# Kernel optimization log

Measured on AMD Instinct MI355X. Metric: run time of the kernel, lower is better.

## Reference

```python
import jax, jax.numpy as jnp
from jax import lax
import numpy as np

N, T, F, H, L, TOPK = 2048, 64, 16, 64, 16, 10


def setup_inputs() -> dict:
    key = jax.random.key(0)
    ks = jax.random.split(key, 12)
    s_ih = 1.0 / np.sqrt(H)
    inp = {
        "x": jax.random.normal(ks[0], (N, T, F), dtype=jnp.float32),
        # GRU params (torch layout: weight_ih_l0 (3H,F), weight_hh_l0 (3H,H))
        "W_ih": jax.random.uniform(ks[1], (3 * H, F), minval=-s_ih, maxval=s_ih),
        "W_hh": jax.random.uniform(ks[2], (3 * H, H), minval=-s_ih, maxval=s_ih),
        "b_ih": jax.random.uniform(ks[3], (3 * H,), minval=-s_ih, maxval=s_ih),
        "b_hh": jax.random.uniform(ks[4], (3 * H,), minval=-s_ih, maxval=s_ih),
        "Wq": jax.random.normal(ks[5], (H, H)) * (1.0 / np.sqrt(H)),
        "Wk": jax.random.normal(ks[6], (H, H)) * (1.0 / np.sqrt(H)),
        "W1": jax.random.normal(ks[7], (F, F)) * (1.0 / np.sqrt(F)),
        "b1": jnp.zeros((F,), jnp.float32),
        "W2": jax.random.normal(ks[8], (1, F)) * (1.0 / np.sqrt(F)),
        "b2": jnp.zeros((1,), jnp.float32),
    }
    return inp


def _gru(x, W_ih, W_hh, b_ih, b_hh):
    # x: (N, T, F) -> hidden states (N, T, H)
    xp = x @ W_ih.T + b_ih  # precompute input gates: (N, T, 3H)

    def step(h, xt):
        gh = h @ W_hh.T + b_hh
        xr, xz, xn = jnp.split(xt, 3, axis=-1)
        hr, hz, hn = jnp.split(gh, 3, axis=-1)
        r = jax.nn.sigmoid(xr + hr)
        z = jax.nn.sigmoid(xz + hz)
        n = jnp.tanh(xn + r * hn)
        h_new = (1.0 - z) * n + z * h
        return h_new, h_new

    h0 = jnp.zeros((x.shape[0], W_hh.shape[1]), x.dtype)
    _, hs = lax.scan(step, h0, jnp.swapaxes(xp, 0, 1))  # (T, N, H)
    return jnp.swapaxes(hs, 0, 1)


def reference(x, W_ih, W_hh, b_ih, b_hh, Wq, Wk, W1, b1, W2, b2):
    n, t, f = x.shape
    h = _gru(x, W_ih, W_hh, b_ih, b_hh)          # (N, T, H)
    queries = h[:, -1, :] @ Wq.T                 # (N, H)
    keys = h[:, -L:, :] @ Wk.T                   # (N, L, H)
    # cross-sample scores: query i vs key (stock m, lag l)
    scores = jnp.einsum("nh,mlh->nml", queries, keys)  # (N, N, L)
    eye = jnp.eye(n, dtype=bool)[:, :, None]
    scores = jnp.where(eye, jnp.float32(-1e9), scores)
    flat = scores.reshape(n, n * L)
    topk_vals, topk_idx = lax.top_k(flat, TOPK)  # order differs from torch sorted=False but math is permutation-invariant
    leader_idx = topk_idx // L                   # (N, k)
    lag_idx = topk_idx % L
    time_idx = t - (L - lag_idx)
    leader_feats = x[leader_idx, time_idx]       # (N, k, F)
    w = jax.nn.softmax(topk_vals, axis=1)
    weighted = jnp.sum(leader_feats * w[..., None], axis=1)  # (N, F)
    hid = jax.nn.leaky_relu(weighted @ W1.T + b1, negative_slope=0.01)
    out = (hid @ W2.T + b2).reshape(-1)          # (N,)
    return out
```

## Files before the change

### kernel.cpp

```cpp
#include <hip/hip_runtime.h>

#define NN 2048
#define TT 64
#define FF 16
#define HH 64
#define LL 16
#define TOPKK 10
#define CAP 960

#define AS 72
#define XAS 40
#define XPS 196

typedef __bf16 bf16x8 __attribute__((ext_vector_type(8)));
typedef float floatx4 __attribute__((ext_vector_type(4)));

union FragCast { uint4 u; bf16x8 b; unsigned short s[8]; };
union Pack4 { unsigned short s[4]; uint2 u; };

__device__ __forceinline__ unsigned short f2bf(float f) {
    unsigned u = __float_as_uint(f);
    return (unsigned short)((u + 0x7fff + ((u >> 16) & 1)) >> 16);
}
__device__ __forceinline__ float bf2f(unsigned short h) {
    return __uint_as_float(((unsigned)h) << 16);
}
__device__ __forceinline__ void split3(float v, unsigned short& a, unsigned short& b, unsigned short& c) {
    a = f2bf(v); float r = v - bf2f(a);
    b = f2bf(r); float r2 = r - bf2f(b);
    c = f2bf(r2);
}
__device__ __forceinline__ float fsigmoid(float x) {
    return __builtin_amdgcn_rcpf(1.f + __builtin_amdgcn_exp2f(-1.442695041f * x));
}
__device__ __forceinline__ float ftanh(float x) {
    return 1.f - 2.f * __builtin_amdgcn_rcpf(1.f + __builtin_amdgcn_exp2f(2.885390082f * x));
}
__device__ __forceinline__ void async_copy16(const void* g, void* l) {
    __builtin_amdgcn_global_load_lds(
        (const __attribute__((address_space(1))) unsigned int*)g,
        (__attribute__((address_space(3))) unsigned int*)l, 16, 0, 0);
}
#define MFMA16(A, B, C) __builtin_amdgcn_mfma_f32_16x16x32_bf16((A), (B), (C), 0, 0, 0)

__global__ __launch_bounds__(256, 2) void gru_kernel(
    const float* __restrict__ x,
    const float* __restrict__ W_ih,
    const float* __restrict__ W_hh,
    const float* __restrict__ b_ih,
    const float* __restrict__ b_hh,
    float* __restrict__ h_tail,
    int* __restrict__ cnt)
{
    __shared__ __attribute__((aligned(16))) unsigned short Asp[2][3][16 * AS];
    __shared__ __attribute__((aligned(16))) unsigned short xa[3][16 * XAS];
    __shared__ __attribute__((aligned(16))) float xp[16 * XPS];
    __shared__ __attribute__((aligned(16))) float x_lds[4 * TT * FF];

    const int t    = threadIdx.x;
    const int wv   = t >> 6;
    const int lane = t & 63;
    const int nh   = lane & 15;
    const int quad = lane >> 4;
    const int n0   = blockIdx.x * 4;

    if (t < 4) cnt[blockIdx.x * 4 + t] = 0;

    {
        const char* src = (const char*)(x + (size_t)n0 * TT * FF);
        char* dst = (char*)x_lds;
#pragma unroll
        for (int i = 0; i < 4; ++i)
            async_copy16(src + i * 4096 + t * 16, dst + i * 4096 + t * 16);
    }
    {
        unsigned* p = (unsigned*)&Asp[0][0][0];
        for (int i = t; i < 2 * 3 * 16 * AS / 2; i += 256) p[i] = 0;
        unsigned* q = (unsigned*)&xa[0][0];
        for (int i = t; i < 3 * 16 * XAS / 2; i += 256) q[i] = 0;
    }

    const int jb = wv * 16 + nh;
    const float brz = b_ih[jb] + b_hh[jb];
    const float bz  = b_ih[64 + jb] + b_hh[64 + jb];
    const float bxn = b_ih[128 + jb];
    const float bhn = b_hh[128 + jb];

    bf16x8 wf[3][2][3];
#pragma unroll
    for (int nt = 0; nt < 3; ++nt) {
        const int gr = (wv + 4 * nt) * 16 + nh;
#pragma unroll
        for (int kc = 0; kc < 2; ++kc) {
            const float* p = W_hh + gr * 64 + kc * 32 + quad * 8;
            FragCast f1, f2, f3;
#pragma unroll
            for (int i = 0; i < 8; ++i) split3(p[i], f1.s[i], f2.s[i], f3.s[i]);
            wf[nt][kc][0] = f1.b; wf[nt][kc][1] = f2.b; wf[nt][kc][2] = f3.b;
        }
    }
    bf16x8 wfi[3][3];
#pragma unroll
    for (int nt = 0; nt < 3; ++nt) {
        const int gr = (wv + 4 * nt) * 16 + nh;
        FragCast f1, f2, f3;
#pragma unroll
        for (int i = 0; i < 8; ++i) {
            const float v = (quad < 2) ? W_ih[gr * 16 + quad * 8 + i] : 0.f;
            split3(v, f1.s[i], f2.s[i], f3.s[i]);
        }
        wfi[nt][0] = f1.b; wfi[nt][1] = f2.b; wfi[nt][2] = f3.b;
    }

    __syncthreads();

    float hprev = 0.f;

    for (int chunk = 0; chunk < 16; ++chunk) {
        {
            const int row = t >> 4, f = t & 15;
            const int p = row & 3, sl = row >> 2;
            const float xv = x_lds[p * (TT * FF) + (chunk * 4 + sl) * FF + f];
            unsigned short a, b, c; split3(xv, a, b, c);
            xa[0][row * XAS + f] = a;
            xa[1][row * XAS + f] = b;
            xa[2][row * XAS + f] = c;
        }
        __syncthreads();
        {
            floatx4 xA0 = {0,0,0,0}, xB0 = {0,0,0,0};
            floatx4 xA1 = {0,0,0,0}, xB1 = {0,0,0,0};
            floatx4 xA2 = {0,0,0,0}, xB2 = {0,0,0,0};
            const int aoff = nh * XAS + quad * 8;
            FragCast a1, a2, a3;
            a1.u = *(const uint4*)&xa[0][aoff];
            a2.u = *(const uint4*)&xa[1][aoff];
            a3.u = *(const uint4*)&xa[2][aoff];
            xA0 = MFMA16(a1.b, wfi[0][0], xA0); xA1 = MFMA16(a1.b, wfi[1][0], xA1); xA2 = MFMA16(a1.b, wfi[2][0], xA2);
            xB0 = MFMA16(a1.b, wfi[0][1], xB0); xB1 = MFMA16(a1.b, wfi[1][1], xB1); xB2 = MFMA16(a1.b, wfi[2][1], xB2);
            xB0 = MFMA16(a2.b, wfi[0][0], xB0); xB1 = MFMA16(a2.b, wfi[1][0], xB1); xB2 = MFMA16(a2.b, wfi[2][0], xB2);
            xA0 = MFMA16(a1.b, wfi[0][2], xA0); xA1 = MFMA16(a1.b, wfi[1][2], xA1); xA2 = MFMA16(a1.b, wfi[2][2], xA2);
            xA0 = MFMA16(a2.b, wfi[0][1], xA0); xA1 = MFMA16(a2.b, wfi[1][1], xA1); xA2 = MFMA16(a2.b, wfi[2][1], xA2);
            xB0 = MFMA16(a3.b, wfi[0][0], xB0); xB1 = MFMA16(a3.b, wfi[1][0], xB1); xB2 = MFMA16(a3.b, wfi[2][0], xB2);
#pragma unroll
            for (int r = 0; r < 4; ++r) {
                const int m = quad * 4 + r;
                xp[m * XPS + (wv + 0) * 16 + nh] = xA0[r] + xB0[r];
                xp[m * XPS + (wv + 4) * 16 + nh] = xA1[r] + xB1[r];
                xp[m * XPS + (wv + 8) * 16 + nh] = xA2[r] + xB2[r];
            }
        }
        __syncthreads();

#pragma unroll
        for (int si = 0; si < 4; ++si) {
            const int step = chunk * 4 + si;
            const int rb = step & 1, wb = rb ^ 1;
            floatx4 aA0 = {0,0,0,0}, aB0 = {0,0,0,0};
            floatx4 aA1 = {0,0,0,0}, aB1 = {0,0,0,0};
            floatx4 aA2 = {0,0,0,0}, aB2 = {0,0,0,0};
#pragma unroll
            for (int kc = 0; kc < 2; ++kc) {
                const int aoff = nh * AS + kc * 32 + quad * 8;
                FragCast a1, a2, a3;
                a1.u = *(const uint4*)&Asp[rb][0][aoff];
                a2.u = *(const uint4*)&Asp[rb][1][aoff];
                a3.u = *(const uint4*)&Asp[rb][2][aoff];
                aA0 = MFMA16(a1.b, wf[0][kc][0], aA0); aA1 = MFMA16(a1.b, wf[1][kc][0], aA1); aA2 = MFMA16(a1.b, wf[2][kc][0], aA2);
                aB0 = MFMA16(a1.b, wf[0][kc][1], aB0); aB1 = MFMA16(a1.b, wf[1][kc][1], aB1); aB2 = MFMA16(a1.b, wf[2][kc][1], aB2);
                aB0 = MFMA16(a2.b, wf[0][kc][0], aB0); aB1 = MFMA16(a2.b, wf[1][kc][0], aB1); aB2 = MFMA16(a2.b, wf[2][kc][0], aB2);
                aA0 = MFMA16(a1.b, wf[0][kc][2], aA0); aA1 = MFMA16(a1.b, wf[1][kc][2], aA1); aA2 = MFMA16(a1.b, wf[2][kc][2], aA2);
                aA0 = MFMA16(a2.b, wf[0][kc][1], aA0); aA1 = MFMA16(a2.b, wf[1][kc][1], aA1); aA2 = MFMA16(a2.b, wf[2][kc][1], aA2);
                aB0 = MFMA16(a3.b, wf[0][kc][0], aB0); aB1 = MFMA16(a3.b, wf[1][kc][0], aB1); aB2 = MFMA16(a3.b, wf[2][kc][0], aB2);
            }
            {
                const int xrow = si * 4 + quad;
                const float xr = xp[xrow * XPS + jb];
                const float xz = xp[xrow * XPS + 64 + jb];
                const float xn = xp[xrow * XPS + 128 + jb];
                const float rgt = fsigmoid((aA0[0] + aB0[0]) + xr + brz);
                const float zgt = fsigmoid((aA1[0] + aB1[0]) + xz + bz);
                const float ngt = ftanh((xn + bxn) + rgt * ((aA2[0] + aB2[0]) + bhn));
                const float h  = (1.f - zgt) * ngt + zgt * hprev;
                hprev = h;
                unsigned short la, lb2, lc; split3(h, la, lb2, lc);
                const int ho = (4 * quad) * AS + jb;
                Asp[wb][0][ho] = la;
                Asp[wb][1][ho] = lb2;
                Asp[wb][2][ho] = lc;
                if (step >= TT - LL)
                    h_tail[((size_t)(n0 + quad) * LL + (step - (TT - LL))) * HH + jb] = h;
            }
            __syncthreads();
        }
    }
}

__global__ __launch_bounds__(256, 2) void prep_kernel(
    const float* __restrict__ h_tail,
    const float* __restrict__ Wk,
    const float* __restrict__ Wq,
    float* __restrict__ Kmat,
    unsigned short* __restrict__ Kh,
    float* __restrict__ Qf,
    unsigned short* __restrict__ Qh)
{
    __shared__ __attribute__((aligned(16))) float Wk_s[64 * 68];
    __shared__ __attribute__((aligned(16))) float Wq_s[64 * 69];
    __shared__ __attribute__((aligned(16))) float h_s[64 * 68];

    const int t = threadIdx.x;
    const size_t rbase = (size_t)blockIdx.x * 64;

#pragma unroll
    for (int k = 0; k < 4; ++k) {
        const int idx = t + k * 256;
        const int j = idx >> 4, ci = idx & 15;
        *(float4*)(h_s + j * 68 + ci * 4) = *(const float4*)(h_tail + (rbase + j) * 64 + ci * 4);
    }
    for (int c = t; c < 1024; c += 256) {
        const int j = c >> 4, ci = c & 15;
        *(float4*)(Wk_s + j * 68 + ((ci ^ (j >> 2)) << 2)) = *(const float4*)(Wk + c * 4);
    }
    for (int c = t; c < 4096; c += 256) {
        const int j = c >> 6, i = c & 63;
        Wq_s[j * 69 + i] = Wq[c];
    }
    __syncthreads();

    const int rg = t >> 4;
    const int cg = t & 15;
    float acc[4][4];
#pragma unroll
    for (int r = 0; r < 4; ++r)
#pragma unroll
        for (int c = 0; c < 4; ++c) acc[r][c] = 0.f;

#pragma unroll
    for (int ci = 0; ci < 16; ++ci) {
        float4 wv[4];
#pragma unroll
        for (int c = 0; c < 4; ++c) {
            const int j = cg * 4 + c;
            wv[c] = *(const float4*)(Wk_s + j * 68 + ((ci ^ cg) << 2));
        }
#pragma unroll
        for (int r = 0; r < 4; ++r) {
            const float4 hv = *(const float4*)(h_s + (rg * 4 + r) * 68 + ci * 4);
#pragma unroll
            for (int c = 0; c < 4; ++c)
                acc[r][c] += hv.x * wv[c].x + hv.y * wv[c].y
                           + hv.z * wv[c].z + hv.w * wv[c].w;
        }
    }
#pragma unroll
    for (int r = 0; r < 4; ++r) {
        const size_t row = rbase + rg * 4 + r;
        float4 o; o.x = acc[r][0]; o.y = acc[r][1]; o.z = acc[r][2]; o.w = acc[r][3];
        *(float4*)(Kmat + row * 64 + cg * 4) = o;
        Pack4 p;
#pragma unroll
        for (int c = 0; c < 4; ++c) p.s[c] = f2bf(acc[r][c]);
        *(uint2*)(Kh + row * 64 + cg * 4) = p.u;
    }

    {
        const int s = t >> 6, j = t & 63;
        const float* hr = h_s + (s * 16 + 15) * 68;
        float a0 = 0.f, a1 = 0.f;
#pragma unroll
        for (int i = 0; i < 64; i += 2) {
            a0 += hr[i] * Wq_s[j * 69 + i];
            a1 += hr[i + 1] * Wq_s[j * 69 + i + 1];
        }
        const float a = a0 + a1;
        const size_t qi = (size_t)(blockIdx.x * 4 + s) * 64 + j;
        Qf[qi] = a;
        Qh[qi] = f2bf(a);
    }
}

__global__ __launch_bounds__(512, 4) void score_kernel(
    const unsigned short* __restrict__ Kh,
    const unsigned short* __restrict__ Qh,
    int* __restrict__ cnt,
    int* __restrict__ ids)
{
    __shared__ float stat_s[8][4][16];
    __shared__ float stat_q[8][4][16];
    __shared__ float th_s[64];

    const int t    = threadIdx.x;
    const int wave = t >> 6;
    const int lane = t & 63;
    const int n    = lane & 15;
    const int quad = lane >> 4;

    const int qgroup = blockIdx.x >> 4;
    const int split  = blockIdx.x & 15;
    const int tile0  = split * 128 + wave * 16;

    FragCast bq[4][2];
#pragma unroll
    for (int qs = 0; qs < 4; ++qs) {
        const int qg = qgroup * 64 + qs * 16 + n;
        bq[qs][0].u = *(const uint4*)(Qh + (size_t)qg * 64 + quad * 8);
        bq[qs][1].u = *(const uint4*)(Qh + (size_t)qg * 64 + 32 + quad * 8);
    }

    float ssum[4] = {0.f,0.f,0.f,0.f}, ssq[4] = {0.f,0.f,0.f,0.f};
    for (int i = 0; i < 8; ++i) {
        const unsigned short* r = Kh + (size_t)((tile0 + i) * 16 + n) * 64;
        FragCast a0, a1;
        a0.u = *(const uint4*)(r + quad * 8);
        a1.u = *(const uint4*)(r + 32 + quad * 8);
#pragma unroll
        for (int qs = 0; qs < 4; ++qs) {
            floatx4 acc = {0.f, 0.f, 0.f, 0.f};
            acc = MFMA16(a0.b, bq[qs][0].b, acc);
            acc = MFMA16(a1.b, bq[qs][1].b, acc);
#pragma unroll
            for (int j = 0; j < 4; ++j) { ssum[qs] += acc[j]; ssq[qs] += acc[j] * acc[j]; }
        }
    }
#pragma unroll
    for (int qs = 0; qs < 4; ++qs) {
        ssum[qs] += __shfl_xor(ssum[qs], 16, 64); ssq[qs] += __shfl_xor(ssq[qs], 16, 64);
        ssum[qs] += __shfl_xor(ssum[qs], 32, 64); ssq[qs] += __shfl_xor(ssq[qs], 32, 64);
    }
    if (lane < 16) {
#pragma unroll
        for (int qs = 0; qs < 4; ++qs) { stat_s[wave][qs][n] = ssum[qs]; stat_q[wave][qs][n] = ssq[qs]; }
    }
    __syncthreads();
    if (t < 64) {
        const int qs = t >> 4, c = t & 15;
        float S = 0.f, S2 = 0.f;
#pragma unroll
        for (int w = 0; w < 8; ++w) { S += stat_s[w][qs][c]; S2 += stat_q[w][qs][c]; }
        const float inv = 1.f / 1024.f;
        const float mu = S * inv;
        float var = S2 * inv - mu * mu;
        var = var > 0.f ? var : 0.f;
        th_s[t] = mu + 2.6f * __fsqrt_rn(var);
    }
    __syncthreads();
    float th[4];
#pragma unroll
    for (int qs = 0; qs < 4; ++qs) th[qs] = th_s[qs * 16 + n];

    {
        FragCast a0, a1, na0, na1;
        const unsigned short* r0 = Kh + (size_t)(tile0 * 16 + n) * 64;
        a0.u = *(const uint4*)(r0 + quad * 8);
        a1.u = *(const uint4*)(r0 + 32 + quad * 8);
        for (int i = 0; i < 16; ++i) {
            if (i + 1 < 16) {
                const unsigned short* r = Kh + (size_t)((tile0 + i + 1) * 16 + n) * 64;
                na0.u = *(const uint4*)(r + quad * 8);
                na1.u = *(const uint4*)(r + 32 + quad * 8);
            }
            const int rowb = (tile0 + i) * 16 + quad * 4;
#pragma unroll
            for (int qs = 0; qs < 4; ++qs) {
                floatx4 acc = {0.f, 0.f, 0.f, 0.f};
                acc = MFMA16(a0.b, bq[qs][0].b, acc);
                acc = MFMA16(a1.b, bq[qs][1].b, acc);
                const int qg = qgroup * 64 + qs * 16 + n;
#pragma unroll
                for (int j = 0; j < 4; ++j) {
                    const float s = acc[j];
                    const int rowid = rowb + j;
                    if (s > th[qs] && (rowid >> 4) != qg) {
                        const int slot = atomicAdd(&cnt[qg], 1);
                        if (slot < CAP) ids[(size_t)qg * CAP + slot] = rowid;
                    }
                }
            }
            a0 = na0; a1 = na1;
        }
    }
}

__global__ __launch_bounds__(512) void final_kernel(
    const float* __restrict__ x,
    const float* __restrict__ Qf,
    const float* __restrict__ Kmat,
    const int* __restrict__ cnt,
    const int* __restrict__ ids,
    const float* __restrict__ W1, const float* __restrict__ b1,
    const float* __restrict__ W2, const float* __restrict__ b2,
    float* __restrict__ out)
{
    const int t    = threadIdx.x;
    const int w    = t >> 6;
    const int lane = t & 63;
    const int grp  = lane >> 4;
    const int sl   = lane & 15;
    const int q    = blockIdx.x * 8 + w;

    const int mc0 = cnt[q];
    const int mc  = mc0 < CAP ? mc0 : CAP;
    const float4 qv = *(const float4*)(Qf + (size_t)q * 64 + sl * 4);
    const int* idq = ids + (size_t)q * CAP;

    float v[TOPKK]; int vid[TOPKK];
#pragma unroll
    for (int r = 0; r < TOPKK; ++r) { v[r] = -3e38f; vid[r] = -1; }
    float vmin = -3e38f; int imin = 0;

    for (int c = grp; c < mc; c += 4) {
        const int id = idq[c];
        const float4 kv = *(const float4*)(Kmat + (size_t)id * 64 + sl * 4);
        float p = qv.x * kv.x + qv.y * kv.y + qv.z * kv.z + qv.w * kv.w;
        p += __shfl_xor(p, 1, 64);
        p += __shfl_xor(p, 2, 64);
        p += __shfl_xor(p, 4, 64);
        p += __shfl_xor(p, 8, 64);
        if (sl == 0 && p > vmin) {
#pragma unroll
            for (int r = 0; r < TOPKK; ++r) if (r == imin) { v[r] = p; vid[r] = id; }
            vmin = v[0]; imin = 0;
#pragma unroll
            for (int r = 1; r < TOPKK; ++r) if (v[r] < vmin) { vmin = v[r]; imin = r; }
        }
    }

    float topv[TOPKK]; int topi[TOPKK];
    unsigned used = 0;
    for (int r = 0; r < TOPKK; ++r) {
        float bv = -3e38f; int bi = -1, bs = -1;
#pragma unroll
        for (int s = 0; s < TOPKK; ++s)
            if (!((used >> s) & 1) && v[s] > bv) { bv = v[s]; bi = vid[s]; bs = s; }
        const float mybv = bv; const int mybi = bi;
#pragma unroll
        for (int st = 16; st <= 32; st <<= 1) {
            const float ov = __shfl_xor(bv, st, 64);
            const int   oi = __shfl_xor(bi, st, 64);
            if (ov > bv || (ov == bv && oi > bi)) { bv = ov; bi = oi; }
        }
        topv[r] = bv; topi[r] = bi;
        if (bs >= 0 && mybv == bv && mybi == bi) used |= (1u << bs);
    }
#pragma unroll
    for (int r = 0; r < TOPKK; ++r) {
        topv[r] = __shfl(topv[r], 0, 64);
        topi[r] = __shfl(topi[r], 0, 64);
    }

    float mx = topv[0];
#pragma unroll
    for (int r = 1; r < TOPKK; ++r) mx = topv[r] > mx ? topv[r] : mx;
    float wgt[TOPKK]; float sw = 0.f;
#pragma unroll
    for (int r = 0; r < TOPKK; ++r) {
        wgt[r] = (topi[r] >= 0) ? __expf(topv[r] - mx) : 0.f;
        sw += wgt[r];
    }
    const float inv = 1.f / sw;

    float4 f0 = {0,0,0,0}, f1 = {0,0,0,0}, f2 = {0,0,0,0}, f3 = {0,0,0,0};
    if (lane < TOPKK && topi[lane] >= 0) {
        const int wi = topi[lane];
        const float* xr = x + ((size_t)(wi >> 4) * TT + 48 + (wi & 15)) * FF;
        const float s = wgt[lane] * inv;
        float4 a = *(const float4*)(xr);
        float4 b = *(const float4*)(xr + 4);
        float4 cc = *(const float4*)(xr + 8);
        float4 d = *(const float4*)(xr + 12);
        f0.x = s * a.x; f0.y = s * a.y; f0.z = s * a.z; f0.w = s * a.w;
        f1.x = s * b.x; f1.y = s * b.y; f1.z = s * b.z; f1.w = s * b.w;
        f2.x = s * cc.x; f2.y = s * cc.y; f2.z = s * cc.z; f2.w = s * cc.w;
        f3.x = s * d.x; f3.y = s * d.y; f3.z = s * d.z; f3.w = s * d.w;
    }
#pragma unroll
    for (int st = 1; st <= 8; st <<= 1) {
        f0.x += __shfl_xor(f0.x, st, 64); f0.y += __shfl_xor(f0.y, st, 64);
        f0.z += __shfl_xor(f0.z, st, 64); f0.w += __shfl_xor(f0.w, st, 64);
        f1.x += __shfl_xor(f1.x, st, 64); f1.y += __shfl_xor(f1.y, st, 64);
        f1.z += __shfl_xor(f1.z, st, 64); f1.w += __shfl_xor(f1.w, st, 64);
        f2.x += __shfl_xor(f2.x, st, 64); f2.y += __shfl_xor(f2.y, st, 64);
        f2.z += __shfl_xor(f2.z, st, 64); f2.w += __shfl_xor(f2.w, st, 64);
        f3.x += __shfl_xor(f3.x, st, 64); f3.y += __shfl_xor(f3.y, st, 64);
        f3.z += __shfl_xor(f3.z, st, 64); f3.w += __shfl_xor(f3.w, st, 64);
    }

    float o = 0.f;
    if (lane < 16) {
        const float* w1r = W1 + lane * 16;
        float hh = b1[lane]
            + f0.x * w1r[0]  + f0.y * w1r[1]  + f0.z * w1r[2]  + f0.w * w1r[3]
            + f1.x * w1r[4]  + f1.y * w1r[5]  + f1.z * w1r[6]  + f1.w * w1r[7]
            + f2.x * w1r[8]  + f2.y * w1r[9]  + f2.z * w1r[10] + f2.w * w1r[11]
            + f3.x * w1r[12] + f3.y * w1r[13] + f3.z * w1r[14] + f3.w * w1r[15];
        hh = hh > 0.f ? hh : 0.01f * hh;
        o = hh * W2[lane];
    }
#pragma unroll
    for (int st = 1; st <= 8; st <<= 1) o += __shfl_xor(o, st, 64);
    if (lane == 0) out[q] = o + b2[0];
}

extern "C" void kernel_launch(void* const* d_in, const int* in_sizes, int n_in,
                              void* d_out, int out_size, void* d_ws, size_t ws_size,
                              hipStream_t stream) {
    const float* x    = (const float*)d_in[0];
    const float* W_ih = (const float*)d_in[1];
    const float* W_hh = (const float*)d_in[2];
    const float* b_ih = (const float*)d_in[3];
    const float* b_hh = (const float*)d_in[4];
    const float* Wq   = (const float*)d_in[5];
    const float* Wk   = (const float*)d_in[6];
    const float* W1   = (const float*)d_in[7];
    const float* b1   = (const float*)d_in[8];
    const float* W2   = (const float*)d_in[9];
    const float* b2   = (const float*)d_in[10];
    float* outp = (float*)d_out;
    (void)ws_size; (void)n_in; (void)in_sizes; (void)out_size;

    float* h_tail        = (float*)d_ws;
    int*   ids           = (int*)d_ws;
    float* Kmat          = h_tail + (size_t)2048 * 1024;
    unsigned short* Kh   = (unsigned short*)(Kmat + (size_t)32768 * 64);
    float* Qf            = (float*)(Kh + (size_t)32768 * 64);
    unsigned short* Qh   = (unsigned short*)(Qf + (size_t)2048 * 64);
    int*   cnt           = (int*)(Qh + (size_t)2048 * 64);

    gru_kernel<<<NN / 4, 256, 0, stream>>>(x, W_ih, W_hh, b_ih, b_hh, h_tail, cnt);
    prep_kernel<<<512, 256, 0, stream>>>(h_tail, Wk, Wq, Kmat, Kh, Qf, Qh);
    score_kernel<<<512, 512, 0, stream>>>(Kh, Qh, cnt, ids);
    final_kernel<<<NN / 8, 512, 0, stream>>>(x, Qf, Kmat, cnt, ids, W1, b1, W2, b2, outp);
}
```

Before: 256.7 us.

## Fuse K/Q projection into GRU kernel and prefetch keys in final kernel

The separate prep kernel is folded into the GRU kernel. The last 16 hidden states stay in a shared-memory arena and the Wk/Wq projections are computed in place, which removes a launch and the h_tail round trip through global memory. The LDS is unified into one 64000-byte arena so the projection can reuse the GRU buffers. This may limit occupancy to the declared two blocks per CU. The final kernel now uses 256-thread blocks and software-prefetches the next candidate's key id and vector to hide gather latency.

Result: no change. 255.2 us (-0.6%).

```diff
diff --git a/kernel.cpp b/kernel.cpp
--- a/kernel.cpp
+++ b/kernel.cpp
@@ -49,13 +49,22 @@
     const float* __restrict__ W_hh,
     const float* __restrict__ b_ih,
     const float* __restrict__ b_hh,
-    float* __restrict__ h_tail,
+    const float* __restrict__ Wk,
+    const float* __restrict__ Wq,
+    float* __restrict__ Kmat,
+    unsigned short* __restrict__ Kh,
+    float* __restrict__ Qf,
+    unsigned short* __restrict__ Qh,
     int* __restrict__ cnt)
 {
-    __shared__ __attribute__((aligned(16))) unsigned short Asp[2][3][16 * AS];
-    __shared__ __attribute__((aligned(16))) unsigned short xa[3][16 * XAS];
-    __shared__ __attribute__((aligned(16))) float xp[16 * XPS];
-    __shared__ __attribute__((aligned(16))) float x_lds[4 * TT * FF];
+    __shared__ __attribute__((aligned(16))) char arena[64000];
+    unsigned short* const Asp0 = (unsigned short*)arena;
+    unsigned short* const xa0  = (unsigned short*)(arena + 13824);
+    float* const xp            = (float*)(arena + 17664);
+    float* const x_lds         = (float*)(arena + 30208);
+    float* const h_keep        = (float*)(arena + 46592);
+#define ASP(b, l, i) Asp0[((b) * 3 + (l)) * (16 * AS) + (i)]
+#define XA(l, i)     xa0[(l) * (16 * XAS) + (i)]
 
     const int t    = threadIdx.x;
     const int wv   = t >> 6;
@@ -74,10 +83,10 @@
             async_copy16(src + i * 4096 + t * 16, dst + i * 4096 + t * 16);
     }
     {
-        unsigned* p = (unsigned*)&Asp[0][0][0];
-        for (int i = t; i < 2 * 3 * 16 * AS / 2; i += 256) p[i] = 0;
-        unsigned* q = (unsigned*)&xa[0][0];
-        for (int i = t; i < 3 * 16 * XAS / 2; i += 256) q[i] = 0;
+        unsigned* p = (unsigned*)Asp0;
+        for (int i = t; i < 3456; i += 256) p[i] = 0;
+        unsigned* q = (unsigned*)xa0;
+        for (int i = t; i < 960; i += 256) q[i] = 0;
     }
 
     const int jb = wv * 16 + nh;
@@ -122,9 +131,9 @@
             const int p = row & 3, sl = row >> 2;
             const float xv = x_lds[p * (TT * FF) + (chunk * 4 + sl) * FF + f];
             unsigned short a, b, c; split3(xv, a, b, c);
-            xa[0][row * XAS + f] = a;
-            xa[1][row * XAS + f] = b;
-            xa[2][row * XAS + f] = c;
+            XA(0, row * XAS + f) = a;
+            XA(1, row * XAS + f) = b;
+            XA(2, row * XAS + f) = c;
         }
         __syncthreads();
         {
@@ -133,9 +142,9 @@
             floatx4 xA2 = {0,0,0,0}, xB2 = {0,0,0,0};
             const int aoff = nh * XAS + quad * 8;
             FragCast a1, a2, a3;
-            a1.u = *(const uint4*)&xa[0][aoff];
-            a2.u = *(const uint4*)&xa[1][aoff];
-            a3.u = *(const uint4*)&xa[2][aoff];
+            a1.u = *(const uint4*)&XA(0, aoff);
+            a2.u = *(const uint4*)&XA(1, aoff);
+            a3.u = *(const uint4*)&XA(2, aoff);
             xA0 = MFMA16(a1.b, wfi[0][0], xA0); xA1 = MFMA16(a1.b, wfi[1][0], xA1); xA2 = MFMA16(a1.b, wfi[2][0], xA2);
             xB0 = MFMA16(a1.b, wfi[0][1], xB0); xB1 = MFMA16(a1.b, wfi[1][1], xB1); xB2 = MFMA16(a1.b, wfi[2][1], xB2);
             xB0 = MFMA16(a2.b, wfi[0][0], xB0); xB1 = MFMA16(a2.b, wfi[1][0], xB1); xB2 = MFMA16(a2.b, wfi[2][0], xB2);
@@ -163,9 +172,9 @@
             for (int kc = 0; kc < 2; ++kc) {
                 const int aoff = nh * AS + kc * 32 + quad * 8;
                 FragCast a1, a2, a3;
-                a1.u = *(const uint4*)&Asp[rb][0][aoff];
-                a2.u = *(const uint4*)&Asp[rb][1][aoff];
-                a3.u = *(const uint4*)&Asp[rb][2][aoff];
+                a1.u = *(const uint4*)&ASP(rb, 0, aoff);
+                a2.u = *(const uint4*)&ASP(rb, 1, aoff);
+                a3.u = *(const uint4*)&ASP(rb, 2, aoff);
                 aA0 = MFMA16(a1.b, wf[0][kc][0], aA0); aA1 = MFMA16(a1.b, wf[1][kc][0], aA1); aA2 = MFMA16(a1.b, wf[2][kc][0], aA2);
                 aB0 = MFMA16(a1.b, wf[0][kc][1], aB0); aB1 = MFMA16(a1.b, wf[1][kc][1], aB1); aB2 = MFMA16(a1.b, wf[2][kc][1], aB2);
                 aB0 = MFMA16(a2.b, wf[0][kc][0], aB0); aB1 = MFMA16(a2.b, wf[1][kc][0], aB1); aB2 = MFMA16(a2.b, wf[2][kc][0], aB2);
@@ -185,39 +194,18 @@
                 hprev = h;
                 unsigned short la, lb2, lc; split3(h, la, lb2, lc);
                 const int ho = (4 * quad) * AS + jb;
-                Asp[wb][0][ho] = la;
-                Asp[wb][1][ho] = lb2;
-                Asp[wb][2][ho] = lc;
+                ASP(wb, 0, ho) = la;
+                ASP(wb, 1, ho) = lb2;
+                ASP(wb, 2, ho) = lc;
                 if (step >= TT - LL)
-                    h_tail[((size_t)(n0 + quad) * LL + (step - (TT - LL))) * HH + jb] = h;
+                    h_keep[(quad * 16 + (step - (TT - LL))) * 68 + jb] = h;
             }
             __syncthreads();
         }
     }
-}
-
-__global__ __launch_bounds__(256, 2) void prep_kernel(
-    const float* __restrict__ h_tail,
-    const float* __restrict__ Wk,
-    const float* __restrict__ Wq,
-    float* __restrict__ Kmat,
-    unsigned short* __restrict__ Kh,
-    float* __restrict__ Qf,
-    unsigned short* __restrict__ Qh)
-{
-    __shared__ __attribute__((aligned(16))) float Wk_s[64 * 68];
-    __shared__ __attribute__((aligned(16))) float Wq_s[64 * 69];
-    __shared__ __attribute__((aligned(16))) float h_s[64 * 68];
-
-    const int t = threadIdx.x;
-    const size_t rbase = (size_t)blockIdx.x * 64;
-
-#pragma unroll
-    for (int k = 0; k < 4; ++k) {
-        const int idx = t + k * 256;
-        const int j = idx >> 4, ci = idx & 15;
-        *(float4*)(h_s + j * 68 + ci * 4) = *(const float4*)(h_tail + (rbase + j) * 64 + ci * 4);
-    }
+
+    float* const Wk_s = (float*)arena;
+    float* const Wq_s = (float*)(arena + 17408);
     for (int c = t; c < 1024; c += 256) {
         const int j = c >> 4, ci = c & 15;
         *(float4*)(Wk_s + j * 68 + ((ci ^ (j >> 2)) << 2)) = *(const float4*)(Wk + c * 4);
@@ -228,45 +216,45 @@
     }
     __syncthreads();
 
-    const int rg = t >> 4;
-    const int cg = t & 15;
-    float acc[4][4];
-#pragma unroll
-    for (int r = 0; r < 4; ++r)
-#pragma unroll
-        for (int c = 0; c < 4; ++c) acc[r][c] = 0.f;
-
-#pragma unroll
-    for (int ci = 0; ci < 16; ++ci) {
-        float4 wv[4];
-#pragma unroll
-        for (int c = 0; c < 4; ++c) {
-            const int j = cg * 4 + c;
-            wv[c] = *(const float4*)(Wk_s + j * 68 + ((ci ^ cg) << 2));
+    {
+        const int rg = t >> 4, cg = t & 15;
+        const size_t rbase = (size_t)blockIdx.x * 64;
+        float acc[4][4];
+#pragma unroll
+        for (int r = 0; r < 4; ++r)
+#pragma unroll
+            for (int c = 0; c < 4; ++c) acc[r][c] = 0.f;
+
+#pragma unroll
+        for (int ci = 0; ci < 16; ++ci) {
+            float4 wvv[4];
+#pragma unroll
+            for (int c = 0; c < 4; ++c) {
+                const int j = cg * 4 + c;
+                wvv[c] = *(const float4*)(Wk_s + j * 68 + ((ci ^ cg) << 2));
+            }
+#pragma unroll
+            for (int r = 0; r < 4; ++r) {
+                const float4 hv = *(const float4*)(h_keep + (rg * 4 + r) * 68 + ci * 4);
+#pragma unroll
+                for (int c = 0; c < 4; ++c)
+                    acc[r][c] += hv.x * wvv[c].x + hv.y * wvv[c].y
+                               + hv.z * wvv[c].z + hv.w * wvv[c].w;
+            }
         }
 #pragma unroll
         for (int r = 0; r < 4; ++r) {
-            const float4 hv = *(const float4*)(h_s + (rg * 4 + r) * 68 + ci * 4);
-#pragma unroll
-            for (int c = 0; c < 4; ++c)
-                acc[r][c] += hv.x * wv[c].x + hv.y * wv[c].y
-                           + hv.z * wv[c].z + hv.w * wv[c].w;
-        }
-    }
-#pragma unroll
-    for (int r = 0; r < 4; ++r) {
-        const size_t row = rbase + rg * 4 + r;
-        float4 o; o.x = acc[r][0]; o.y = acc[r][1]; o.z = acc[r][2]; o.w = acc[r][3];
-        *(float4*)(Kmat + row * 64 + cg * 4) = o;
-        Pack4 p;
-#pragma unroll
-        for (int c = 0; c < 4; ++c) p.s[c] = f2bf(acc[r][c]);
-        *(uint2*)(Kh + row * 64 + cg * 4) = p.u;
-    }
-
-    {
+            const size_t row = rbase + rg * 4 + r;
+            float4 o; o.x = acc[r][0]; o.y = acc[r][1]; o.z = acc[r][2]; o.w = acc[r][3];
+            *(float4*)(Kmat + row * 64 + cg * 4) = o;
+            Pack4 p;
+#pragma unroll
+            for (int c = 0; c < 4; ++c) p.s[c] = f2bf(acc[r][c]);
+            *(uint2*)(Kh + row * 64 + cg * 4) = p.u;
+        }
+
         const int s = t >> 6, j = t & 63;
-        const float* hr = h_s + (s * 16 + 15) * 68;
+        const float* hr = h_keep + (s * 16 + 15) * 68;
         float a0 = 0.f, a1 = 0.f;
 #pragma unroll
         for (int i = 0; i < 64; i += 2) {
@@ -278,6 +266,8 @@
         Qf[qi] = a;
         Qh[qi] = f2bf(a);
     }
+#undef ASP
+#undef XA
 }
 
 __global__ __launch_bounds__(512, 4) void score_kernel(
@@ -382,7 +372,7 @@
     }
 }
 
-__global__ __launch_bounds__(512) void final_kernel(
+__global__ __launch_bounds__(256) void final_kernel(
     const float* __restrict__ x,
     const float* __restrict__ Qf,
     const float* __restrict__ Kmat,
@@ -397,7 +387,7 @@
     const int lane = t & 63;
     const int grp  = lane >> 4;
     const int sl   = lane & 15;
-    const int q    = blockIdx.x * 8 + w;
+    const int q    = blockIdx.x * 4 + w;
 
     const int mc0 = cnt[q];
     const int mc  = mc0 < CAP ? mc0 : CAP;
@@ -409,21 +399,30 @@
     for (int r = 0; r < TOPKK; ++r) { v[r] = -3e38f; vid[r] = -1; }
     float vmin = -3e38f; int imin = 0;
 
+    int idc = -1; float4 kvc = {0, 0, 0, 0};
+    if (grp < mc) {
+        idc = idq[grp];
+        kvc = *(const float4*)(Kmat + (size_t)idc * 64 + sl * 4);
+    }
     for (int c = grp; c < mc; c += 4) {
-        const int id = idq[c];
-        const float4 kv = *(const float4*)(Kmat + (size_t)id * 64 + sl * 4);
-        float p = qv.x * kv.x + qv.y * kv.y + qv.z * kv.z + qv.w * kv.w;
+        int idn = -1; float4 kvn = {0, 0, 0, 0};
+        if (c + 4 < mc) {
+            idn = idq[c + 4];
+            kvn = *(const float4*)(Kmat + (size_t)idn * 64 + sl * 4);
+        }
+        float p = qv.x * kvc.x + qv.y * kvc.y + qv.z * kvc.z + qv.w * kvc.w;
         p += __shfl_xor(p, 1, 64);
         p += __shfl_xor(p, 2, 64);
         p += __shfl_xor(p, 4, 64);
         p += __shfl_xor(p, 8, 64);
         if (sl == 0 && p > vmin) {
 #pragma unroll
-            for (int r = 0; r < TOPKK; ++r) if (r == imin) { v[r] = p; vid[r] = id; }
+            for (int r = 0; r < TOPKK; ++r) if (r == imin) { v[r] = p; vid[r] = idc; }
             vmin = v[0]; imin = 0;
 #pragma unroll
             for (int r = 1; r < TOPKK; ++r) if (v[r] < vmin) { vmin = v[r]; imin = r; }
         }
+        idc = idn; kvc = kvn;
     }
 
     float topv[TOPKK]; int topi[TOPKK];
@@ -519,16 +518,15 @@
     float* outp = (float*)d_out;
     (void)ws_size; (void)n_in; (void)in_sizes; (void)out_size;
 
-    float* h_tail        = (float*)d_ws;
     int*   ids           = (int*)d_ws;
-    float* Kmat          = h_tail + (size_t)2048 * 1024;
+    float* Kmat          = (float*)d_ws + (size_t)2048 * 1024;
     unsigned short* Kh   = (unsigned short*)(Kmat + (size_t)32768 * 64);
     float* Qf            = (float*)(Kh + (size_t)32768 * 64);
     unsigned short* Qh   = (unsigned short*)(Qf + (size_t)2048 * 64);
     int*   cnt           = (int*)(Qh + (size_t)2048 * 64);
 
-    gru_kernel<<<NN / 4, 256, 0, stream>>>(x, W_ih, W_hh, b_ih, b_hh, h_tail, cnt);
-    prep_kernel<<<512, 256, 0, stream>>>(h_tail, Wk, Wq, Kmat, Kh, Qf, Qh);
+    gru_kernel<<<NN / 4, 256, 0, stream>>>(x, W_ih, W_hh, b_ih, b_hh, Wk, Wq,
+                                           Kmat, Kh, Qf, Qh, cnt);
     score_kernel<<<512, 512, 0, stream>>>(Kh, Qh, cnt, ids);
-    final_kernel<<<NN / 8, 512, 0, stream>>>(x, Qf, Kmat, cnt, ids, W1, b1, W2, b2, outp);
-}
+    final_kernel<<<NN / 4, 256, 0, stream>>>(x, Qf, Kmat, cnt, ids, W1, b1, W2, b2, outp);
+}
```
